# Kernel tuning notes

Hardware: AMD Instinct MI355X
Metric: run time of the kernel (lower is better)

The kernel has to match this reference:

```python
import jax, jax.numpy as jnp
import numpy as np

B, C, N, H, W = 4, 3, 262144, 1024, 1024
HW = H * W
GROUP_COLS = ([0], [1, 2], [1])  # AREA, (GRAY_HEIGHT, VARIANCE_LEVEL), GRAY_HEIGHT


def setup_inputs() -> dict:
    key = jax.random.key(0)
    ks = jax.random.split(key, 10)
    rng = np.random.default_rng(0)
    # parent[i] < i (topological order); root (index 0) points to dummy node N.
    u = rng.random((B, C, N - 1))
    par = (u * np.arange(1, N, dtype=np.float64)).astype(np.int32)
    parent = jnp.asarray(np.concatenate([np.full((B, C, 1), N, np.int32), par], axis=-1))
    # gray-level residue (level(node) - level(parent)) >= 0 for a max-tree
    residue = jax.random.uniform(ks[0], (B, C, N), dtype=jnp.float32) * 8.0
    attrs = jax.random.normal(ks[1], (B, C, N, 3), dtype=jnp.float32)
    pixel_node = jax.random.randint(ks[2], (B, C, HW), 0, N, dtype=jnp.int32)
    # torch init: uniform(-1e-5, 1e-5) weights, bias = 1.0
    W0 = jax.random.uniform(ks[3], (1,), minval=-1e-5, maxval=1e-5, dtype=jnp.float32)
    W1 = jax.random.uniform(ks[4], (2,), minval=-1e-5, maxval=1e-5, dtype=jnp.float32)
    W2 = jax.random.uniform(ks[5], (1,), minval=-1e-5, maxval=1e-5, dtype=jnp.float32)
    b0 = jnp.ones((1,), jnp.float32)
    b1 = jnp.ones((1,), jnp.float32)
    b2 = jnp.ones((1,), jnp.float32)
    return {"attrs": attrs, "residue": residue, "W0": W0, "W1": W1, "W2": W2,
            "b0": b0, "b1": b1, "b2": b2, "parent": parent, "pixel_node": pixel_node}


def _tree_prefix(parent, contrib):
    """f(n) = sum of contrib over n and all its ancestors, via pointer jumping.
    parent: (..., N) int32 in [0, N] (N = dummy root sentinel); contrib: (..., N)."""
    n = contrib.shape[-1]
    acc = jnp.concatenate([contrib, jnp.zeros(contrib.shape[:-1] + (1,), contrib.dtype)], -1)
    ptr = jnp.concatenate([parent, jnp.full(parent.shape[:-1] + (1,), n, parent.dtype)], -1)
    for _ in range(int(np.ceil(np.log2(n + 1)))):
        acc = acc + jnp.take_along_axis(acc, ptr, axis=-1)
        ptr = jnp.take_along_axis(ptr, ptr, axis=-1)
    return acc[..., :n]


def reference(attrs, residue, W0, W1, W2, b0, b1, b2, parent, pixel_node):
    Ws, bs = (W0, W1, W2), (b0, b1, b2)
    outs = []
    for cols, Wg, bg in zip(GROUP_COLS, Ws, bs):
        feats = attrs[..., jnp.array(cols)]              # (B,C,N,Fg)
        s = jax.nn.sigmoid(feats @ Wg + bg)              # per-node score (B,C,N)
        f = _tree_prefix(parent, s * residue)            # connected filter (B,C,N)
        outs.append(jnp.take_along_axis(f, pixel_node, axis=-1))  # (B,C,HW)
    y = jnp.stack(outs, axis=2)                          # (B,C,G,HW)
    return y.reshape(B, C * len(GROUP_COLS), H, W)
```

## Files before the change

### kernel.cpp

```cpp
#include <hip/hip_runtime.h>

#define NNODES 262144
#define HWPIX  1048576
#define BC     12
#define NGROUP 3

__device__ __forceinline__ float sigm(float x) {
    return 1.0f / (1.0f + __expf(-x));
}

__global__ __launch_bounds__(256) void k_contrib(
    const float* __restrict__ attrs,
    const float* __restrict__ residue,
    const int*   __restrict__ parent,
    const float* __restrict__ W0, const float* __restrict__ W1,
    const float* __restrict__ W2, const float* __restrict__ b0,
    const float* __restrict__ b1, const float* __restrict__ b2,
    float4* __restrict__ contrib)
{
    const float w0 = W0[0], w10 = W1[0], w11 = W1[1], w2 = W2[0];
    const float c0 = b0[0], c1 = b1[0], c2 = b2[0];

    int t = blockIdx.x * blockDim.x + threadIdx.x;
    const float4* a4 = (const float4*)attrs + (size_t)t * 3;
    float4 A = a4[0], Bv = a4[1], Cv = a4[2];
    float4 r  = ((const float4*)residue)[t];
    int4  par = ((const int4*)parent)[t];

    float4 o0, o1, o2, o3;
    o0.x = r.x * sigm(A.x * w0 + c0);
    o0.y = r.x * sigm(A.y * w10 + A.z * w11 + c1);
    o0.z = r.x * sigm(A.y * w2 + c2);
    o0.w = __int_as_float(par.x);
    o1.x = r.y * sigm(A.w * w0 + c0);
    o1.y = r.y * sigm(Bv.x * w10 + Bv.y * w11 + c1);
    o1.z = r.y * sigm(Bv.x * w2 + c2);
    o1.w = __int_as_float(par.y);
    o2.x = r.z * sigm(Bv.z * w0 + c0);
    o2.y = r.z * sigm(Bv.w * w10 + Cv.x * w11 + c1);
    o2.z = r.z * sigm(Bv.w * w2 + c2);
    o2.w = __int_as_float(par.z);
    o3.x = r.w * sigm(Cv.y * w0 + c0);
    o3.y = r.w * sigm(Cv.z * w10 + Cv.w * w11 + c1);
    o3.z = r.w * sigm(Cv.z * w2 + c2);
    o3.w = __int_as_float(par.w);

    float4* dst = contrib + (size_t)t * 4;
    dst[0] = o0; dst[1] = o1; dst[2] = o2; dst[3] = o3;
}

__global__ __launch_bounds__(256) void k_scan(
    const float4* __restrict__ contrib,
    float4* __restrict__ f)
{
    int idx = blockIdx.x * blockDim.x + threadIdx.x;
    int bcbase = idx & ~(NNODES - 1);
    float4 c = contrib[idx];
    float fx = c.x, fy = c.y, fz = c.z;
    int j = __float_as_int(c.w);
    while (j != NNODES) {
        float4 cj = contrib[bcbase + j];
        fx += cj.x; fy += cj.y; fz += cj.z;
        j = __float_as_int(cj.w);
    }
    f[idx] = make_float4(fx, fy, fz, 0.0f);
}

__global__ __launch_bounds__(256) void k_gather(
    const float4* __restrict__ f,
    const int*    __restrict__ pixel_node,
    float* __restrict__ out)
{
    int t = blockIdx.x * blockDim.x + threadIdx.x;
    size_t gp = (size_t)t * 4;
    int bc = (int)(gp >> 20);
    int p  = (int)(gp & (HWPIX - 1));
    int4 pn = ((const int4*)pixel_node)[t];
    const float4* fb = f + ((size_t)bc << 18);
    float4 f0 = fb[pn.x], f1 = fb[pn.y], f2 = fb[pn.z], f3 = fb[pn.w];
    float* o = out + (size_t)bc * 3 * HWPIX + p;
    *(float4*)(o)             = make_float4(f0.x, f1.x, f2.x, f3.x);
    *(float4*)(o + HWPIX)     = make_float4(f0.y, f1.y, f2.y, f3.y);
    *(float4*)(o + 2 * HWPIX) = make_float4(f0.z, f1.z, f2.z, f3.z);
}

extern "C" void kernel_launch(void* const* d_in, const int* in_sizes, int n_in,
                              void* d_out, int out_size, void* d_ws, size_t ws_size,
                              hipStream_t stream) {
    const float* attrs      = (const float*)d_in[0];
    const float* residue    = (const float*)d_in[1];
    const float* W0         = (const float*)d_in[2];
    const float* W1         = (const float*)d_in[3];
    const float* W2         = (const float*)d_in[4];
    const float* b0         = (const float*)d_in[5];
    const float* b1         = (const float*)d_in[6];
    const float* b2         = (const float*)d_in[7];
    const int*   parent     = (const int*)d_in[8];
    const int*   pixel_node = (const int*)d_in[9];
    float* out = (float*)d_out;

    const size_t total_nodes = (size_t)BC * NNODES;
    float4* contrib = (float4*)d_ws;
    float4* fbuf    = contrib + total_nodes;

    {
        int threads = (int)(total_nodes / 4);
        k_contrib<<<threads / 256, 256, 0, stream>>>(
            attrs, residue, parent, W0, W1, W2, b0, b1, b2, contrib);
    }
    {
        int threads = (int)total_nodes;
        k_scan<<<threads / 256, 256, 0, stream>>>(contrib, fbuf);
    }
    {
        int threads = (int)((size_t)BC * HWPIX / 4);
        k_gather<<<threads / 256, 256, 0, stream>>>(fbuf, pixel_node, out);
    }
}
```

Before: 431.2 us.

## Split tree-prefix scan into index-range chunks reusing finished ancestor results

The per-node ancestor walk now runs in four launches over growing index ranges. Nodes in later chunks stop walking once they reach an ancestor below the chunk's lower bound and add that ancestor's already computed prefix from the output table. This shortens the long dependent pointer chases of the original walk-to-root. The scan and gather kernels also use an XCD-aware block swizzle for L2 locality, and gather processes 8 pixels per thread. The cost is extra launches and serialization between chunks.

Result: faster. 377.8 us (-12.4%).

```diff
diff --git a/kernel.cpp b/kernel.cpp
--- a/kernel.cpp
+++ b/kernel.cpp
@@ -3,10 +3,14 @@
 #define NNODES 262144
 #define HWPIX  1048576
 #define BC     12
-#define NGROUP 3
 
 __device__ __forceinline__ float sigm(float x) {
     return 1.0f / (1.0f + __expf(-x));
+}
+
+__device__ __forceinline__ int xcd_swizzle(int orig, int nwg) {
+    int q = nwg >> 3;
+    return (orig & 7) * q + (orig >> 3);
 }
 
 __global__ __launch_bounds__(256) void k_contrib(
@@ -49,21 +53,36 @@
     dst[0] = o0; dst[1] = o1; dst[2] = o2; dst[3] = o3;
 }
 
-__global__ __launch_bounds__(256) void k_scan(
+__global__ __launch_bounds__(256) void k_scan_chunk(
     const float4* __restrict__ contrib,
-    float4* __restrict__ f)
+    float4* __restrict__ ftab,
+    int lo, int cnt)
 {
-    int idx = blockIdx.x * blockDim.x + threadIdx.x;
-    int bcbase = idx & ~(NNODES - 1);
-    float4 c = contrib[idx];
+    int w = xcd_swizzle(blockIdx.x, gridDim.x);
+    int bpt = cnt >> 8;
+    int bc  = w / bpt;
+    int i   = lo + (w % bpt) * 256 + threadIdx.x;
+    int bcbase = bc << 18;
+
+    float4 c = contrib[bcbase + i];
     float fx = c.x, fy = c.y, fz = c.z;
     int j = __float_as_int(c.w);
-    while (j != NNODES) {
-        float4 cj = contrib[bcbase + j];
-        fx += cj.x; fy += cj.y; fz += cj.z;
-        j = __float_as_int(cj.w);
+    if (lo == 0) {
+        while (j != NNODES) {
+            float4 cj = contrib[bcbase + j];
+            fx += cj.x; fy += cj.y; fz += cj.z;
+            j = __float_as_int(cj.w);
+        }
+    } else {
+        while (j >= lo) {
+            float4 cj = contrib[bcbase + j];
+            fx += cj.x; fy += cj.y; fz += cj.z;
+            j = __float_as_int(cj.w);
+        }
+        float4 fp = ftab[bcbase + j];
+        fx += fp.x; fy += fp.y; fz += fp.z;
     }
-    f[idx] = make_float4(fx, fy, fz, 0.0f);
+    ftab[bcbase + i] = make_float4(fx, fy, fz, 0.0f);
 }
 
 __global__ __launch_bounds__(256) void k_gather(
@@ -71,17 +90,22 @@
     const int*    __restrict__ pixel_node,
     float* __restrict__ out)
 {
-    int t = blockIdx.x * blockDim.x + threadIdx.x;
-    size_t gp = (size_t)t * 4;
+    int w = xcd_swizzle(blockIdx.x, gridDim.x);
+    size_t gp = (size_t)w * 2048 + (size_t)threadIdx.x * 8;
     int bc = (int)(gp >> 20);
     int p  = (int)(gp & (HWPIX - 1));
-    int4 pn = ((const int4*)pixel_node)[t];
+    const int4* pn4 = (const int4*)(pixel_node + gp);
+    int4 pa = pn4[0], pb = pn4[1];
     const float4* fb = f + ((size_t)bc << 18);
-    float4 f0 = fb[pn.x], f1 = fb[pn.y], f2 = fb[pn.z], f3 = fb[pn.w];
+    float4 f0 = fb[pa.x], f1 = fb[pa.y], f2 = fb[pa.z], f3 = fb[pa.w];
+    float4 f4 = fb[pb.x], f5 = fb[pb.y], f6 = fb[pb.z], f7 = fb[pb.w];
     float* o = out + (size_t)bc * 3 * HWPIX + p;
-    *(float4*)(o)             = make_float4(f0.x, f1.x, f2.x, f3.x);
-    *(float4*)(o + HWPIX)     = make_float4(f0.y, f1.y, f2.y, f3.y);
-    *(float4*)(o + 2 * HWPIX) = make_float4(f0.z, f1.z, f2.z, f3.z);
+    *(float4*)(o)                 = make_float4(f0.x, f1.x, f2.x, f3.x);
+    *(float4*)(o + 4)             = make_float4(f4.x, f5.x, f6.x, f7.x);
+    *(float4*)(o + HWPIX)         = make_float4(f0.y, f1.y, f2.y, f3.y);
+    *(float4*)(o + HWPIX + 4)     = make_float4(f4.y, f5.y, f6.y, f7.y);
+    *(float4*)(o + 2 * HWPIX)     = make_float4(f0.z, f1.z, f2.z, f3.z);
+    *(float4*)(o + 2 * HWPIX + 4) = make_float4(f4.z, f5.z, f6.z, f7.z);
 }
 
 extern "C" void kernel_launch(void* const* d_in, const int* in_sizes, int n_in,
@@ -101,19 +125,20 @@
 
     const size_t total_nodes = (size_t)BC * NNODES;
     float4* contrib = (float4*)d_ws;
-    float4* fbuf    = contrib + total_nodes;
+    float4* ftab    = contrib + total_nodes;
+
+    k_contrib<<<(int)(total_nodes / 4 / 256), 256, 0, stream>>>(
+        attrs, residue, parent, W0, W1, W2, b0, b1, b2, contrib);
 
     {
-        int threads = (int)(total_nodes / 4);
-        k_contrib<<<threads / 256, 256, 0, stream>>>(
-            attrs, residue, parent, W0, W1, W2, b0, b1, b2, contrib);
+        int bounds[5] = {0, 4096, 16384, 65536, NNODES};
+        for (int k = 0; k < 4; ++k) {
+            int lo = bounds[k], cnt = bounds[k + 1] - bounds[k];
+            int nblk = cnt / 256 * BC;
+            k_scan_chunk<<<nblk, 256, 0, stream>>>(contrib, ftab, lo, cnt);
+        }
     }
-    {
-        int threads = (int)total_nodes;
-        k_scan<<<threads / 256, 256, 0, stream>>>(contrib, fbuf);
-    }
-    {
-        int threads = (int)((size_t)BC * HWPIX / 4);
-        k_gather<<<threads / 256, 256, 0, stream>>>(fbuf, pixel_node, out);
-    }
+
+    k_gather<<<(int)((size_t)BC * HWPIX / 2048), 256, 0, stream>>>(
+        ftab, pixel_node, out);
 }
```
